# Performance work log

Hardware: AMD Instinct MI355X
Metric: run time of the kernel (lower is better)

Reference implementation:

```python
import jax, jax.numpy as jnp
import numpy as np

B, L_IN, L_CTX, DIM, HEADS = 2, 1536, 256, 1024, 16
HEAD_DIM = DIM // HEADS  # 64
EPS = 1e-6


def _rmsnorm(x, w):
    # RMSNorm over the full inner_dim, matching QKNorm(inner_dim)
    return x * jax.lax.rsqrt(jnp.mean(x * x, axis=-1, keepdims=True) + EPS) * w


def _rope(x, cos, sin):
    # x: (b, n, h, d); cos/sin: (n, d//2); rotate adjacent pairs
    xp = x.reshape(x.shape[:-1] + (HEAD_DIM // 2, 2))
    x1, x2 = xp[..., 0], xp[..., 1]
    c = cos[None, :, None, :]
    s = sin[None, :, None, :]
    out = jnp.stack([x1 * c - x2 * s, x1 * s + x2 * c], axis=-1)
    return out.reshape(x.shape)


def setup_inputs():
    key = jax.random.key(0)
    ks = jax.random.split(key, 12)
    std = 0.02
    inp = jax.random.normal(ks[0], (B, L_IN, DIM), jnp.float32)
    ctx = jax.random.normal(ks[1], (B, L_CTX, DIM), jnp.float32)
    # rope tables over concatenated sequence (context first, then input)
    n = L_CTX + L_IN
    half = HEAD_DIM // 2
    inv_freq = 1.0 / (10000.0 ** (np.arange(half, dtype=np.float32) / half))
    ang = np.arange(n, dtype=np.float32)[:, None] * inv_freq[None, :]
    cos = jnp.asarray(np.cos(ang))
    sin = jnp.asarray(np.sin(ang))
    return {
        "input": inp,
        "context": ctx,
        "cos": cos,
        "sin": sin,
        "Wqkv_in": jax.random.normal(ks[2], (DIM, 3 * DIM), jnp.float32) * std,
        "bqkv_in": jnp.zeros((3 * DIM,), jnp.float32),
        "Wqkv_ctx": jax.random.normal(ks[3], (DIM, 3 * DIM), jnp.float32) * std,
        "bqkv_ctx": jnp.zeros((3 * DIM,), jnp.float32),
        "qw_in": jnp.ones((DIM,), jnp.float32),
        "kw_in": jnp.ones((DIM,), jnp.float32),
        "qw_ctx": jnp.ones((DIM,), jnp.float32),
        "kw_ctx": jnp.ones((DIM,), jnp.float32),
        "Wo_in": jax.random.normal(ks[4], (DIM, DIM), jnp.float32) * std,
        "bo_in": jnp.zeros((DIM,), jnp.float32),
        "Wo_ctx": jax.random.normal(ks[5], (DIM, DIM), jnp.float32) * std,
        "bo_ctx": jnp.zeros((DIM,), jnp.float32),
        "attn_mask": jnp.ones((B, L_CTX), jnp.int32),
    }


def reference(input, context, cos, sin, Wqkv_in, bqkv_in, Wqkv_ctx, bqkv_ctx,
              qw_in, kw_in, qw_ctx, kw_ctx, Wo_in, bo_in, Wo_ctx, bo_ctx, attn_mask):
    # fused QKV projections, then chunk
    qi, ki, vi = jnp.split(input @ Wqkv_in + bqkv_in, 3, axis=-1)
    qc, kc, vc = jnp.split(context @ Wqkv_ctx + bqkv_ctx, 3, axis=-1)
    # QKNorm (RMSNorm over inner_dim)
    qi, ki = _rmsnorm(qi, qw_in), _rmsnorm(ki, kw_in)
    qc, kc = _rmsnorm(qc, qw_ctx), _rmsnorm(kc, kw_ctx)
    # concat context-first, split heads: (b, n, h, d)
    heads = lambda x: x.reshape(B, -1, HEADS, HEAD_DIM)
    q = heads(jnp.concatenate([qc, qi], axis=1))
    k = heads(jnp.concatenate([kc, ki], axis=1))
    v = heads(jnp.concatenate([vc, vi], axis=1))
    # RoPE on q, k (v untouched)
    q = _rope(q, cos, sin)
    k = _rope(k, cos, sin)
    # SDPA: (b, h, n, d)
    q, k, v = (x.transpose(0, 2, 1, 3) for x in (q, k, v))
    scale = HEAD_DIM ** -0.5
    scores = jnp.einsum('bhqd,bhkd->bhqk', q, k) * scale
    full_mask = jnp.concatenate(
        [attn_mask.astype(bool), jnp.ones((B, L_IN), bool)], axis=1)
    scores = jnp.where(full_mask[:, None, None, :], scores,
                       jnp.finfo(scores.dtype).min)
    attn = jax.nn.softmax(scores, axis=-1)
    out = jnp.einsum('bhqk,bhkd->bhqd', attn, v)
    out = out.transpose(0, 2, 1, 3).reshape(B, L_CTX + L_IN, DIM)
    input_output = out[:, L_CTX:, :] @ Wo_in + bo_in
    context_output = out[:, :L_CTX, :] @ Wo_ctx + bo_ctx
    return input_output, context_output
```

## Files before the change

### kernel.cpp

```cpp
#include <hip/hip_runtime.h>
#include <stdint.h>

#define DIMSZ 1024
#define NHEADS 16
#define HD 64
#define BB 2
#define L_IN 1536
#define L_CTX 256
#define NTOT 1792
#define MROWS 3584
#define NT64 (NTOT / 64)

typedef __attribute__((ext_vector_type(8))) short bf16x8;
typedef __attribute__((ext_vector_type(4))) float f32x4;
typedef __attribute__((ext_vector_type(16))) float f32x16;

__device__ inline unsigned short f2bf(float f) {
    union { float f; unsigned u; } v; v.f = f;
    unsigned r = v.u + 0x7fffu + ((v.u >> 16) & 1u);
    return (unsigned short)(r >> 16);
}
__device__ inline float bf2f(unsigned short u) {
    union { float f; unsigned u; } v; v.u = ((unsigned)u) << 16; return v.f;
}
__device__ inline float fexp2(float x) {
    float r;
    asm("v_exp_f32 %0, %1" : "=v"(r) : "v"(x));
    return r;
}

__device__ inline f32x4 zero4() {
    f32x4 v;
    #pragma unroll
    for (int i = 0; i < 4; i++) v[i] = 0.f;
    return v;
}
__device__ inline f32x16 zero16() {
    f32x16 v;
    #pragma unroll
    for (int i = 0; i < 16; i++) v[i] = 0.f;
    return v;
}

#define GLL16(g, l) __builtin_amdgcn_global_load_lds( \
    (const __attribute__((address_space(1))) unsigned int*)(g), \
    (__attribute__((address_space(3))) unsigned int*)(l), 16, 0, 0)

__global__ __launch_bounds__(256) void prep_kernel(
    const float* __restrict__ input, const float* __restrict__ context,
    unsigned short* __restrict__ Abuf,
    const float* __restrict__ Wq_in,  unsigned short* __restrict__ WqT_in,
    const float* __restrict__ Wq_ctx, unsigned short* __restrict__ WqT_ctx,
    const float* __restrict__ Wo_in,  unsigned short* __restrict__ WoT_in,
    const float* __restrict__ Wo_ctx, unsigned short* __restrict__ WoT_ctx)
{
    __shared__ unsigned short sm[64][65];
    int blk = blockIdx.x;
    int t = threadIdx.x;
    if (blk < 3584) {
        int e = (blk * 256 + t) * 4;
        int row = e >> 10, c = e & 1023;
        int b = row / NTOT, ln = row % NTOT;
        const float* src = (ln < L_CTX)
            ? context + ((size_t)b * L_CTX + ln) * 1024 + c
            : input   + ((size_t)b * L_IN + (ln - L_CTX)) * 1024 + c;
        float4 v = *(const float4*)src;
        ushort4 o; o.x = f2bf(v.x); o.y = f2bf(v.y); o.z = f2bf(v.z); o.w = f2bf(v.w);
        *(ushort4*)(Abuf + e) = o;
        return;
    }
    const float* W; unsigned short* Wt; int N; int tb;
    if (blk < 4352)      { W = Wq_in;  Wt = WqT_in;  N = 3072; tb = blk - 3584; }
    else if (blk < 5120) { W = Wq_ctx; Wt = WqT_ctx; N = 3072; tb = blk - 4352; }
    else if (blk < 5376) { W = Wo_in;  Wt = WoT_in;  N = 1024; tb = blk - 5120; }
    else                 { W = Wo_ctx; Wt = WoT_ctx; N = 1024; tb = blk - 5376; }
    int k0 = (tb & 15) * 64, n0 = (tb >> 4) * 64;
    #pragma unroll
    for (int i = 0; i < 4; i++) {
        int r = (t >> 4) + i * 16, c = (t & 15) * 4;
        float4 v = *(const float4*)(W + (size_t)(k0 + r) * N + n0 + c);
        sm[r][c] = f2bf(v.x); sm[r][c + 1] = f2bf(v.y);
        sm[r][c + 2] = f2bf(v.z); sm[r][c + 3] = f2bf(v.w);
    }
    __syncthreads();
    int rn = t & 63, kc = (t >> 6) * 16;
    unsigned short* dst = Wt + (size_t)(n0 + rn) * 1024 + k0 + kc;
    #pragma unroll
    for (int q = 0; q < 4; q++) {
        ushort4 o;
        o.x = sm[kc + q * 4 + 0][rn]; o.y = sm[kc + q * 4 + 1][rn];
        o.z = sm[kc + q * 4 + 2][rn]; o.w = sm[kc + q * 4 + 3][rn];
        *(ushort4*)(dst + q * 4) = o;
    }
}

template<int NLD, bool OUT_BF16, bool IS_QKV>
__global__ __launch_bounds__(256, 4) void gemm2(
    const unsigned short* __restrict__ A,
    const unsigned short* __restrict__ Wt_in, const unsigned short* __restrict__ Wt_ctx,
    const float* __restrict__ bias_in, const float* __restrict__ bias_ctx,
    void* __restrict__ out_in_, void* __restrict__ out_ctx_)
{
    __shared__ __align__(16) unsigned short Asm[128 * 64];
    __shared__ __align__(16) unsigned short Bsm[128 * 64];
    const int rt = blockIdx.x, n0 = blockIdx.y * 128;
    const int b = rt / 14, lrt = rt % 14;
    const bool is_ctx = lrt < 2;
    const unsigned short* Wt = is_ctx ? Wt_ctx : Wt_in;
    const float* bias = is_ctx ? bias_ctx : bias_in;
    const int t = threadIdx.x, lane = t & 63, wid = t >> 6;
    const int wr = wid >> 1, wc = wid & 1;
    const int g4 = lane >> 4, l16 = lane & 15;

    const char* asrc[4]; const char* bsrc[4];
    #pragma unroll
    for (int j = 0; j < 4; j++) {
        int o = t * 16 + j * 4096;
        int row = o >> 7;
        int cb = (o & 127) ^ ((row & 7) << 4);
        asrc[j] = (const char*)A  + ((size_t)(rt * 128 + row)) * 2048 + cb;
        bsrc[j] = (const char*)Wt + ((size_t)(n0 + row)) * 2048 + cb;
    }

    f32x4 acc[4][4];
    #pragma unroll
    for (int mi = 0; mi < 4; mi++)
        #pragma unroll
        for (int ni = 0; ni < 4; ni++) acc[mi][ni] = zero4();

    for (int ks = 0; ks < 16; ks++) {
        __syncthreads();
        #pragma unroll
        for (int j = 0; j < 4; j++) {
            int o = t * 16 + j * 4096;
            GLL16(asrc[j], (char*)Asm + o);
            GLL16(bsrc[j], (char*)Bsm + o);
            asrc[j] += 128; bsrc[j] += 128;
        }
        __syncthreads();
        #pragma unroll
        for (int kk = 0; kk < 2; kk++) {
            bf16x8 a[4], bgf[4];
            #pragma unroll
            for (int mi = 0; mi < 4; mi++) {
                int row = wr * 64 + mi * 16 + l16;
                int byte = row * 128 + ((kk * 64 + g4 * 16) ^ ((row & 7) << 4));
                a[mi] = *(const bf16x8*)((const char*)Asm + byte);
            }
            #pragma unroll
            for (int ni = 0; ni < 4; ni++) {
                int col = wc * 64 + ni * 16 + l16;
                int byte = col * 128 + ((kk * 64 + g4 * 16) ^ ((col & 7) << 4));
                bgf[ni] = *(const bf16x8*)((const char*)Bsm + byte);
            }
            #pragma unroll
            for (int mi = 0; mi < 4; mi++)
                #pragma unroll
                for (int ni = 0; ni < 4; ni++)
                    acc[mi][ni] = __builtin_amdgcn_mfma_f32_16x16x32_bf16(
                        a[mi], bgf[ni], acc[mi][ni], 0, 0, 0);
        }
    }

    char* optr; size_t orow0;
    if constexpr (IS_QKV) {
        optr = (char*)out_in_; orow0 = (size_t)rt * 128;
    } else {
        if (is_ctx) { optr = (char*)out_ctx_; orow0 = (size_t)b * 256 + lrt * 128; }
        else        { optr = (char*)out_in_;  orow0 = (size_t)b * 1536 + (lrt - 2) * 128; }
    }
    #pragma unroll
    for (int mi = 0; mi < 4; mi++)
        #pragma unroll
        for (int ni = 0; ni < 4; ni++) {
            int col = n0 + wc * 64 + ni * 16 + l16;
            float bv = bias[col];
            #pragma unroll
            for (int r = 0; r < 4; r++) {
                size_t row = orow0 + wr * 64 + mi * 16 + g4 * 4 + r;
                float val = acc[mi][ni][r] + bv;
                if constexpr (OUT_BF16)
                    ((unsigned short*)optr)[row * NLD + col] = f2bf(val);
                else
                    ((float*)optr)[row * NLD + col] = val;
            }
        }
}

__global__ __launch_bounds__(256) void norm_rope_kernel(
    const unsigned short* __restrict__ qkv,
    const float* __restrict__ qw_in, const float* __restrict__ kw_in,
    const float* __restrict__ qw_ctx, const float* __restrict__ kw_ctx,
    const float* __restrict__ cosT, const float* __restrict__ sinT,
    unsigned short* __restrict__ Q, unsigned short* __restrict__ K,
    unsigned short* __restrict__ Vt)
{
    const float QSC = 0.125f * 1.44269504088896f;
    int bn = blockIdx.x;
    int b = bn / NTOT, n = bn % NTOT;
    int t = threadIdx.x;
    const unsigned short* row = qkv + (size_t)bn * 3072;
    ushort4 qu = *(const ushort4*)(row + t * 4);
    ushort4 ku = *(const ushort4*)(row + 1024 + t * 4);
    ushort4 vu = *(const ushort4*)(row + 2048 + t * 4);
    float q0f = bf2f(qu.x), q1f = bf2f(qu.y), q2f = bf2f(qu.z), q3f = bf2f(qu.w);
    float k0f = bf2f(ku.x), k1f = bf2f(ku.y), k2f = bf2f(ku.z), k3f = bf2f(ku.w);
    float sq = q0f * q0f + q1f * q1f + q2f * q2f + q3f * q3f;
    float sk = k0f * k0f + k1f * k1f + k2f * k2f + k3f * k3f;
    #pragma unroll
    for (int m = 1; m < 64; m <<= 1) { sq += __shfl_xor(sq, m); sk += __shfl_xor(sk, m); }
    __shared__ float redq[4], redk[4];
    int lane = t & 63, w = t >> 6;
    if (lane == 0) { redq[w] = sq; redk[w] = sk; }
    __syncthreads();
    sq = redq[0] + redq[1] + redq[2] + redq[3];
    sk = redk[0] + redk[1] + redk[2] + redk[3];
    float rsq = rsqrtf(sq * (1.f / 1024.f) + 1e-6f);
    float rsk = rsqrtf(sk * (1.f / 1024.f) + 1e-6f);
    bool is_ctx = (n < L_CTX);
    const float* qw = is_ctx ? qw_ctx : qw_in;
    const float* kw = is_ctx ? kw_ctx : kw_in;
    int col = t * 4;
    int h = col >> 6, d = col & 63;
    float c0 = cosT[n * 32 + (d >> 1)],     s0 = sinT[n * 32 + (d >> 1)];
    float c1 = cosT[n * 32 + (d >> 1) + 1], s1 = sinT[n * 32 + (d >> 1) + 1];
    size_t base = (((size_t)(b * NHEADS + h)) * NTOT + n) * HD + d;
    {
        float x0 = q0f * rsq * qw[col],     x1 = q1f * rsq * qw[col + 1];
        float x2 = q2f * rsq * qw[col + 2], x3 = q3f * rsq * qw[col + 3];
        float y0 = x0 * c0 - x1 * s0, y1 = x0 * s0 + x1 * c0;
        float y2 = x2 * c1 - x3 * s1, y3 = x2 * s1 + x3 * c1;
        ushort4 o; o.x = f2bf(y0 * QSC); o.y = f2bf(y1 * QSC);
        o.z = f2bf(y2 * QSC); o.w = f2bf(y3 * QSC);
        *(ushort4*)(Q + base) = o;
    }
    {
        float x0 = k0f * rsk * kw[col],     x1 = k1f * rsk * kw[col + 1];
        float x2 = k2f * rsk * kw[col + 2], x3 = k3f * rsk * kw[col + 3];
        float y0 = x0 * c0 - x1 * s0, y1 = x0 * s0 + x1 * c0;
        float y2 = x2 * c1 - x3 * s1, y3 = x2 * s1 + x3 * c1;
        ushort4 o; o.x = f2bf(y0); o.y = f2bf(y1); o.z = f2bf(y2); o.w = f2bf(y3);
        *(ushort4*)(K + base) = o;
    }
    size_t vb = ((size_t)(b * NHEADS + h)) * HD;
    Vt[(vb + d + 0) * NTOT + n] = vu.x;
    Vt[(vb + d + 1) * NTOT + n] = vu.y;
    Vt[(vb + d + 2) * NTOT + n] = vu.z;
    Vt[(vb + d + 3) * NTOT + n] = vu.w;
}

__global__ __launch_bounds__(256) void attn_kernel(
    const unsigned short* __restrict__ Q, const unsigned short* __restrict__ K,
    const unsigned short* __restrict__ Vt, const int* __restrict__ mask,
    unsigned short* __restrict__ Ob)
{
    __shared__ __align__(16) char smem[33792];
    float* mbias = (float*)(smem + 32768);
    int bh = blockIdx.x;
    int b = bh >> 4, h = bh & 15;
    int t = threadIdx.x, lane = t & 63, wid = t >> 6;
    int g = lane >> 5, lq = lane & 31;
    int q0 = blockIdx.y * 128 + wid * 32;

    const unsigned short* Qp = Q + (size_t)bh * NTOT * HD;
    const char* Kbase = (const char*)(K + (size_t)bh * NTOT * HD);
    const char* Vbase = (const char*)(Vt + (size_t)bh * HD * NTOT);

    int srow = wid * 8 + (lane >> 3);
    int srcb = ((lane & 7) * 16) ^ ((lane >> 3) << 4);
    const char* ks0 = Kbase + (size_t)srow * 128 + srcb;
    const char* ks1 = ks0 + 32 * 128;
    const char* vs0 = Vbase + (size_t)srow * (NTOT * 2) + srcb;
    const char* vs1 = vs0 + (size_t)32 * (NTOT * 2);
    const int sdst = wid * 1024 + lane * 16;

    auto stage = [&](int bufbase, int tt) {
        GLL16(ks0 + (size_t)tt * 8192, smem + bufbase + sdst);
        GLL16(ks1 + (size_t)tt * 8192, smem + bufbase + 4096 + sdst);
        GLL16(vs0 + (size_t)tt * 128,  smem + bufbase + 8192 + sdst);
        GLL16(vs1 + (size_t)tt * 128,  smem + bufbase + 8192 + 4096 + sdst);
    };

    stage(0, 0);
    if (t < L_CTX) mbias[t] = mask[b * L_CTX + t] ? 0.f : -1e30f;

    bf16x8 qf[4];
    #pragma unroll
    for (int kk = 0; kk < 4; kk++)
        qf[kk] = *(const bf16x8*)(Qp + (size_t)(q0 + lq) * HD + kk * 16 + g * 8);

    f32x16 oacc0 = zero16(), oacc1 = zero16();
    float mrun = -1e30f, denom = 0.f;
    const int ksw = (lq & 7) << 4;

    auto pack2 = [&](const f32x16& p, bf16x8* pfo) {
        #pragma unroll
        for (int kk = 0; kk < 2; kk++) {
            unsigned a1, b1, a2, b2;
            asm("v_cvt_pk_bf16_f32 %0, %1, %2" : "=v"(a1) : "v"(p[8 * kk + 0]), "v"(p[8 * kk + 1]));
            asm("v_cvt_pk_bf16_f32 %0, %1, %2" : "=v"(a2) : "v"(p[8 * kk + 2]), "v"(p[8 * kk + 3]));
            asm("v_cvt_pk_bf16_f32 %0, %1, %2" : "=v"(b1) : "v"(p[8 * kk + 4]), "v"(p[8 * kk + 5]));
            asm("v_cvt_pk_bf16_f32 %0, %1, %2" : "=v"(b2) : "v"(p[8 * kk + 6]), "v"(p[8 * kk + 7]));
            union { unsigned u[4]; bf16x8 v; } pu;
#if __has_builtin(__builtin_amdgcn_permlane32_swap)
            auto r1 = __builtin_amdgcn_permlane32_swap((int)a1, (int)b1, false, false);
            auto r2 = __builtin_amdgcn_permlane32_swap((int)a2, (int)b2, false, false);
            pu.u[0] = (unsigned)r1[0];
            pu.u[1] = (unsigned)r2[0];
            pu.u[2] = (unsigned)r1[1];
            pu.u[3] = (unsigned)r2[1];
#else
            unsigned sa1 = __shfl_xor(a1, 32), sb1 = __shfl_xor(b1, 32);
            unsigned sa2 = __shfl_xor(a2, 32), sb2 = __shfl_xor(b2, 32);
            pu.u[0] = g ? sb1 : a1;
            pu.u[1] = g ? sb2 : a2;
            pu.u[2] = g ? b1 : sa1;
            pu.u[3] = g ? b2 : sa2;
#endif
            pfo[kk] = pu.v;
        }
    };

    auto compute = [&](const char* bufK, const char* bufV, int kv0, bool msk) {
        f32x16 st0 = zero16(), st1 = zero16();
        #pragma unroll
        for (int kk = 0; kk < 4; kk++) {
            int off = (kk * 32 + g * 16) ^ ksw;
            bf16x8 kf0 = *(const bf16x8*)(bufK + lq * 128 + off);
            bf16x8 kf1 = *(const bf16x8*)(bufK + (lq + 32) * 128 + off);
            st0 = __builtin_amdgcn_mfma_f32_32x32x16_bf16(kf0, qf[kk], st0, 0, 0, 0);
            st1 = __builtin_amdgcn_mfma_f32_32x32x16_bf16(kf1, qf[kk], st1, 0, 0, 0);
        }
        if (msk) {
            #pragma unroll
            for (int r = 0; r < 16; r++) {
                int crow = (r & 3) + 8 * (r >> 2) + 4 * g;
                st0[r] += mbias[kv0 + crow];
                st1[r] += mbias[kv0 + 32 + crow];
            }
        }
        float mx[16];
        #pragma unroll
        for (int r = 0; r < 16; r++) mx[r] = fmaxf(st0[r], st1[r]);
        #pragma unroll
        for (int off = 8; off >= 1; off >>= 1) {
            #pragma unroll
            for (int r = 0; r < 8; r++)
                if (r < off) mx[r] = fmaxf(mx[r], mx[r + off]);
        }
        float tmax = fmaxf(mx[0], __shfl_xor(mx[0], 32));
        if (!__all(tmax - mrun <= 8.f)) {
            float mnew = fmaxf(mrun, tmax);
            float corr = fexp2(mrun - mnew);
            denom *= corr; mrun = mnew;
            #pragma unroll
            for (int i = 0; i < 16; i++) { oacc0[i] *= corr; oacc1[i] *= corr; }
        }
        #pragma unroll
        for (int r = 0; r < 16; r++) st0[r] = fexp2(st0[r] - mrun);
        #pragma unroll
        for (int r = 0; r < 16; r++) st1[r] = fexp2(st1[r] - mrun);
        float sm[16];
        #pragma unroll
        for (int r = 0; r < 16; r++) sm[r] = st0[r] + st1[r];
        #pragma unroll
        for (int off = 8; off >= 1; off >>= 1) {
            #pragma unroll
            for (int r = 0; r < 8; r++)
                if (r < off) sm[r] = sm[r] + sm[r + off];
        }
        denom += sm[0] + __shfl_xor(sm[0], 32);
        bf16x8 pf[4];
        pack2(st0, pf);
        pack2(st1, pf + 2);
        #pragma unroll
        for (int kk = 0; kk < 4; kk++) {
            int off = (kk * 32 + g * 16) ^ ksw;
            bf16x8 va = *(const bf16x8*)(bufV + lq * 128 + off);
            bf16x8 vb = *(const bf16x8*)(bufV + (lq + 32) * 128 + off);
            oacc0 = __builtin_amdgcn_mfma_f32_32x32x16_bf16(va, pf[kk], oacc0, 0, 0, 0);
            oacc1 = __builtin_amdgcn_mfma_f32_32x32x16_bf16(vb, pf[kk], oacc1, 0, 0, 0);
        }
    };

    __syncthreads();

    #pragma unroll 1
    for (int tt = 0; tt < NT64; tt++) {
        int curb = (tt & 1) * 16384;
        if (tt + 1 < NT64) stage(16384 - curb, tt + 1);
        compute(smem + curb, smem + curb + 8192, tt * 64, tt < 4);
        __syncthreads();
    }

    float inv = 1.0f / denom;
    int n = q0 + lq;
    size_t obase = ((size_t)(b * NTOT + n)) * DIMSZ + h * HD;
    #pragma unroll
    for (int r = 0; r < 16; r++) {
        int d = (r & 3) + 8 * (r >> 2) + 4 * g;
        Ob[obase + d] = f2bf(oacc0[r] * inv);
        Ob[obase + 32 + d] = f2bf(oacc1[r] * inv);
    }
}

extern "C" void kernel_launch(void* const* d_in, const int* in_sizes, int n_in,
                              void* d_out, int out_size, void* d_ws, size_t ws_size,
                              hipStream_t stream) {
    const float* input    = (const float*)d_in[0];
    const float* context  = (const float*)d_in[1];
    const float* cosT     = (const float*)d_in[2];
    const float* sinT     = (const float*)d_in[3];
    const float* Wqkv_in  = (const float*)d_in[4];
    const float* bqkv_in  = (const float*)d_in[5];
    const float* Wqkv_ctx = (const float*)d_in[6];
    const float* bqkv_ctx = (const float*)d_in[7];
    const float* qw_in    = (const float*)d_in[8];
    const float* kw_in    = (const float*)d_in[9];
    const float* qw_ctx   = (const float*)d_in[10];
    const float* kw_ctx   = (const float*)d_in[11];
    const float* Wo_in    = (const float*)d_in[12];
    const float* bo_in    = (const float*)d_in[13];
    const float* Wo_ctx   = (const float*)d_in[14];
    const float* bo_ctx   = (const float*)d_in[15];
    const int*   mask     = (const int*)d_in[16];

    char* ws = (char*)d_ws;
    unsigned short* WoT_in  = (unsigned short*)(ws);
    unsigned short* WoT_ctx = (unsigned short*)(ws + 2097152);
    unsigned short* qkvb    = (unsigned short*)(ws + 4194304);
    char* U = ws + 26214400;
    unsigned short* Abuf    = (unsigned short*)(U);
    unsigned short* WqT_in  = (unsigned short*)(U + 7340032);
    unsigned short* WqT_ctx = (unsigned short*)(U + 13631488);
    unsigned short* Qb      = (unsigned short*)(U);
    unsigned short* Kb      = (unsigned short*)(U + 7340032);
    unsigned short* Vt      = (unsigned short*)(U + 14680064);
    unsigned short* Ob      = (unsigned short*)(U + 22020096);
    if (ws_size < 64749568) return;

    float* out_in  = (float*)d_out;
    float* out_ctx = out_in + (size_t)BB * L_IN * DIMSZ;

    prep_kernel<<<5632, 256, 0, stream>>>(
        input, context, Abuf,
        Wqkv_in, WqT_in, Wqkv_ctx, WqT_ctx, Wo_in, WoT_in, Wo_ctx, WoT_ctx);

    gemm2<3072, true, true><<<dim3(28, 24), 256, 0, stream>>>(
        Abuf, WqT_in, WqT_ctx, bqkv_in, bqkv_ctx, qkvb, qkvb);

    norm_rope_kernel<<<MROWS, 256, 0, stream>>>(
        qkvb, qw_in, kw_in, qw_ctx, kw_ctx, cosT, sinT, Qb, Kb, Vt);

    attn_kernel<<<dim3(BB * NHEADS, NTOT / 128), 256, 0, stream>>>(
        Qb, Kb, Vt, mask, Ob);

    gemm2<1024, false, false><<<dim3(28, 8), 256, 0, stream>>>(
        Ob, WoT_in, WoT_ctx, bo_in, bo_ctx, out_in, out_ctx);
}
```

Before: 166.4 us.

## Add triple-buffered async-LDS QKV GEMM with swizzled shared memory

Replaces the QKV projection GEMM with a new kernel that stages A and W tiles into a three-slot LDS ring using direct global-to-LDS loads, prefetching two K-tiles ahead and using vmcnt waits plus raw barriers. LDS addresses use an XOR swizzle to reduce bank conflicts for the MFMA fragment reads. The aim is to overlap global memory latency with the MFMA work. In exchange it uses 48KB of LDS per block, which may limit occupancy. The loop also issues redundant wrap-around prefetches for the last tiles.

```diff
diff --git a/kernel.cpp b/kernel.cpp
--- a/kernel.cpp
+++ b/kernel.cpp
@@ -92,6 +92,97 @@
         o.z = sm[kc + q * 4 + 2][rn]; o.w = sm[kc + q * 4 + 3][rn];
         *(ushort4*)(dst + q * 4) = o;
     }
+}
+
+__global__ __launch_bounds__(256, 4) void gemm3(
+    const unsigned short* __restrict__ A,
+    const unsigned short* __restrict__ Wt_in, const unsigned short* __restrict__ Wt_ctx,
+    const float* __restrict__ bias_in, const float* __restrict__ bias_ctx,
+    unsigned short* __restrict__ out)
+{
+    __shared__ __align__(16) char smem[49152];
+    const int rt = blockIdx.x, n0 = blockIdx.y * 128;
+    const bool is_ctx = (rt % 14) < 2;
+    const unsigned short* Wt = is_ctx ? Wt_ctx : Wt_in;
+    const float* bias = is_ctx ? bias_ctx : bias_in;
+    const int t = threadIdx.x, lane = t & 63, wid = t >> 6;
+    const int wr = wid >> 1, wc = wid & 1;
+    const int g4 = lane >> 4, l16 = lane & 15;
+
+    const char* asrc[2]; const char* bsrc[2];
+    int ldst[2];
+    #pragma unroll
+    for (int j = 0; j < 2; j++) {
+        int o = t * 16 + j * 4096;
+        int row = o >> 6;
+        int cb = (o & 63) ^ ((row & 3) << 4);
+        asrc[j] = (const char*)A  + ((size_t)(rt * 128 + row)) * 2048 + cb;
+        bsrc[j] = (const char*)Wt + ((size_t)(n0 + row)) * 2048 + cb;
+        ldst[j] = o;
+    }
+
+    f32x4 acc[4][4];
+    #pragma unroll
+    for (int mi = 0; mi < 4; mi++)
+        #pragma unroll
+        for (int ni = 0; ni < 4; ni++) acc[mi][ni] = zero4();
+
+    auto stage = [&](int kt, int buf) {
+        char* base = smem + buf * 16384;
+        #pragma unroll
+        for (int j = 0; j < 2; j++) {
+            GLL16(asrc[j] + kt * 64, base + ldst[j]);
+            GLL16(bsrc[j] + kt * 64, base + 8192 + ldst[j]);
+        }
+    };
+
+    stage(0, 0);
+    stage(1, 1);
+
+    int bufc = 0;
+    #pragma unroll 1
+    for (int kt = 0; kt < 32; kt++) {
+        int bufs = bufc + 2; if (bufs >= 3) bufs -= 3;
+        stage((kt + 2) & 31, bufs);
+        asm volatile("s_waitcnt vmcnt(4)" ::: "memory");
+        __builtin_amdgcn_s_barrier();
+        const char* base = smem + bufc * 16384;
+        bf16x8 a[4], bgf[4];
+        #pragma unroll
+        for (int mi = 0; mi < 4; mi++) {
+            int row = wr * 64 + mi * 16 + l16;
+            int byte = row * 64 + ((g4 * 16) ^ ((row & 3) << 4));
+            a[mi] = *(const bf16x8*)(base + byte);
+        }
+        #pragma unroll
+        for (int ni = 0; ni < 4; ni++) {
+            int row = wc * 64 + ni * 16 + l16;
+            int byte = 8192 + row * 64 + ((g4 * 16) ^ ((row & 3) << 4));
+            bgf[ni] = *(const bf16x8*)(base + byte);
+        }
+        #pragma unroll
+        for (int mi = 0; mi < 4; mi++)
+            #pragma unroll
+            for (int ni = 0; ni < 4; ni++)
+                acc[mi][ni] = __builtin_amdgcn_mfma_f32_16x16x32_bf16(
+                    a[mi], bgf[ni], acc[mi][ni], 0, 0, 0);
+        __builtin_amdgcn_s_barrier();
+        bufc = bufc + 1; if (bufc >= 3) bufc -= 3;
+    }
+    asm volatile("s_waitcnt vmcnt(0)" ::: "memory");
+
+    #pragma unroll
+    for (int mi = 0; mi < 4; mi++)
+        #pragma unroll
+        for (int ni = 0; ni < 4; ni++) {
+            int col = n0 + wc * 64 + ni * 16 + l16;
+            float bv = bias[col];
+            #pragma unroll
+            for (int r = 0; r < 4; r++) {
+                size_t row = (size_t)rt * 128 + wr * 64 + mi * 16 + g4 * 4 + r;
+                out[row * 3072 + col] = f2bf(acc[mi][ni][r] + bv);
+            }
+        }
 }
 
 template<int NLD, bool OUT_BF16, bool IS_QKV>
@@ -446,8 +537,8 @@
         input, context, Abuf,
         Wqkv_in, WqT_in, Wqkv_ctx, WqT_ctx, Wo_in, WoT_in, Wo_ctx, WoT_ctx);
 
-    gemm2<3072, true, true><<<dim3(28, 24), 256, 0, stream>>>(
-        Abuf, WqT_in, WqT_ctx, bqkv_in, bqkv_ctx, qkvb, qkvb);
+    gemm3<<<dim3(28, 24), 256, 0, stream>>>(
+        Abuf, WqT_in, WqT_ctx, bqkv_in, bqkv_ctx, qkvb);
 
     norm_rope_kernel<<<MROWS, 256, 0, stream>>>(
         qkvb, qw_in, kw_in, qw_ctx, kw_ctx, cosT, sinT, Qb, Kb, Vt);
```

After: 154.2 us. -7.3%, faster.

## Triple-buffer GEMM LDS tiles with async global-to-LDS prefetch two steps ahead

Applied to the files above, without the earlier changes.

Restructures both GEMMs to use a 3-stage LDS ring of 32-wide K tiles, issuing direct global-to-LDS loads two iterations ahead and waiting with vmcnt instead of a full sync per tile. The aim is to overlap memory latency with MFMA work, which the previous load-sync-compute loop serialized. It halves K per step (more barriers, fewer MFMAs per sync) and raises LDS use to 48KB, which may limit occupancy. It also issues redundant wrap-around prefetches at the tail.

```diff
diff --git a/kernel.cpp b/kernel.cpp
--- a/kernel.cpp
+++ b/kernel.cpp
@@ -95,14 +95,13 @@
 }
 
 template<int NLD, bool OUT_BF16, bool IS_QKV>
-__global__ __launch_bounds__(256, 4) void gemm2(
+__global__ __launch_bounds__(256, 4) void gemm3(
     const unsigned short* __restrict__ A,
     const unsigned short* __restrict__ Wt_in, const unsigned short* __restrict__ Wt_ctx,
     const float* __restrict__ bias_in, const float* __restrict__ bias_ctx,
     void* __restrict__ out_in_, void* __restrict__ out_ctx_)
 {
-    __shared__ __align__(16) unsigned short Asm[128 * 64];
-    __shared__ __align__(16) unsigned short Bsm[128 * 64];
+    __shared__ __align__(16) char smem[49152];
     const int rt = blockIdx.x, n0 = blockIdx.y * 128;
     const int b = rt / 14, lrt = rt % 14;
     const bool is_ctx = lrt < 2;
@@ -112,14 +111,16 @@
     const int wr = wid >> 1, wc = wid & 1;
     const int g4 = lane >> 4, l16 = lane & 15;
 
-    const char* asrc[4]; const char* bsrc[4];
-    #pragma unroll
-    for (int j = 0; j < 4; j++) {
+    const char* asrc[2]; const char* bsrc[2];
+    int ldst[2];
+    #pragma unroll
+    for (int j = 0; j < 2; j++) {
         int o = t * 16 + j * 4096;
-        int row = o >> 7;
-        int cb = (o & 127) ^ ((row & 7) << 4);
+        int row = o >> 6;
+        int cb = (o & 63) ^ ((row & 3) << 4);
         asrc[j] = (const char*)A  + ((size_t)(rt * 128 + row)) * 2048 + cb;
         bsrc[j] = (const char*)Wt + ((size_t)(n0 + row)) * 2048 + cb;
+        ldst[j] = o;
     }
 
     f32x4 acc[4][4];
@@ -128,39 +129,49 @@
         #pragma unroll
         for (int ni = 0; ni < 4; ni++) acc[mi][ni] = zero4();
 
-    for (int ks = 0; ks < 16; ks++) {
-        __syncthreads();
-        #pragma unroll
-        for (int j = 0; j < 4; j++) {
-            int o = t * 16 + j * 4096;
-            GLL16(asrc[j], (char*)Asm + o);
-            GLL16(bsrc[j], (char*)Bsm + o);
-            asrc[j] += 128; bsrc[j] += 128;
-        }
-        __syncthreads();
-        #pragma unroll
-        for (int kk = 0; kk < 2; kk++) {
-            bf16x8 a[4], bgf[4];
-            #pragma unroll
-            for (int mi = 0; mi < 4; mi++) {
-                int row = wr * 64 + mi * 16 + l16;
-                int byte = row * 128 + ((kk * 64 + g4 * 16) ^ ((row & 7) << 4));
-                a[mi] = *(const bf16x8*)((const char*)Asm + byte);
-            }
-            #pragma unroll
-            for (int ni = 0; ni < 4; ni++) {
-                int col = wc * 64 + ni * 16 + l16;
-                int byte = col * 128 + ((kk * 64 + g4 * 16) ^ ((col & 7) << 4));
-                bgf[ni] = *(const bf16x8*)((const char*)Bsm + byte);
-            }
-            #pragma unroll
-            for (int mi = 0; mi < 4; mi++)
-                #pragma unroll
-                for (int ni = 0; ni < 4; ni++)
-                    acc[mi][ni] = __builtin_amdgcn_mfma_f32_16x16x32_bf16(
-                        a[mi], bgf[ni], acc[mi][ni], 0, 0, 0);
-        }
-    }
+    auto stage = [&](int kt, int buf) {
+        char* base = smem + buf * 16384;
+        #pragma unroll
+        for (int j = 0; j < 2; j++) {
+            GLL16(asrc[j] + kt * 64, base + ldst[j]);
+            GLL16(bsrc[j] + kt * 64, base + 8192 + ldst[j]);
+        }
+    };
+
+    stage(0, 0);
+    stage(1, 1);
+
+    int bufc = 0;
+    #pragma unroll 1
+    for (int kt = 0; kt < 32; kt++) {
+        int bufs = bufc + 2; if (bufs >= 3) bufs -= 3;
+        stage((kt + 2) & 31, bufs);
+        asm volatile("s_waitcnt vmcnt(8)" ::: "memory");
+        __builtin_amdgcn_s_barrier();
+        const char* base = smem + bufc * 16384;
+        bf16x8 a[4], bgf[4];
+        #pragma unroll
+        for (int mi = 0; mi < 4; mi++) {
+            int row = wr * 64 + mi * 16 + l16;
+            int byte = row * 64 + ((g4 * 16) ^ ((row & 3) << 4));
+            a[mi] = *(const bf16x8*)(base + byte);
+        }
+        #pragma unroll
+        for (int ni = 0; ni < 4; ni++) {
+            int row = wc * 64 + ni * 16 + l16;
+            int byte = 8192 + row * 64 + ((g4 * 16) ^ ((row & 3) << 4));
+            bgf[ni] = *(const bf16x8*)(base + byte);
+        }
+        #pragma unroll
+        for (int mi = 0; mi < 4; mi++)
+            #pragma unroll
+            for (int ni = 0; ni < 4; ni++)
+                acc[mi][ni] = __builtin_amdgcn_mfma_f32_16x16x32_bf16(
+                    a[mi], bgf[ni], acc[mi][ni], 0, 0, 0);
+        __builtin_amdgcn_s_barrier();
+        bufc = bufc + 1; if (bufc >= 3) bufc -= 3;
+    }
+    asm volatile("s_waitcnt vmcnt(0)" ::: "memory");
 
     char* optr; size_t orow0;
     if constexpr (IS_QKV) {
@@ -446,7 +457,7 @@
         input, context, Abuf,
         Wqkv_in, WqT_in, Wqkv_ctx, WqT_ctx, Wo_in, WoT_in, Wo_ctx, WoT_ctx);
 
-    gemm2<3072, true, true><<<dim3(28, 24), 256, 0, stream>>>(
+    gemm3<3072, true, true><<<dim3(28, 24), 256, 0, stream>>>(
         Abuf, WqT_in, WqT_ctx, bqkv_in, bqkv_ctx, qkvb, qkvb);
 
     norm_rope_kernel<<<MROWS, 256, 0, stream>>>(
@@ -455,6 +466,6 @@
     attn_kernel<<<dim3(BB * NHEADS, NTOT / 128), 256, 0, stream>>>(
         Qb, Kb, Vt, mask, Ob);
 
-    gemm2<1024, false, false><<<dim3(28, 8), 256, 0, stream>>>(
+    gemm3<1024, false, false><<<dim3(28, 8), 256, 0, stream>>>(
         Ob, WoT_in, WoT_ctx, bo_in, bo_ctx, out_in, out_ctx);
 }
```

After: 143.5 us. 1.16x faster.
